# Kernel optimization log

Measured on AMD Instinct MI355X. Metric: run time of the kernel, lower is better.

Reference implementation:

```python
import jax, jax.numpy as jnp
import numpy as np

B, C, NB, H, W = 4, 128, 4, 256, 256
BT = C // NB  # bottleneck channels = 32
BN1_EPS, BN2_EPS = 1e-5, 1e-3


def setup_inputs() -> dict:
    key = jax.random.key(0)
    ks = jax.random.split(key, 16)
    x = jax.random.normal(ks[0], (B, C, H, W), dtype=jnp.float32)
    w1 = jax.random.normal(ks[1], (BT, C), dtype=jnp.float32) * 0.1
    bn1_gamma = 1.0 + 0.1 * jax.random.normal(ks[2], (BT,), dtype=jnp.float32)
    bn1_beta = 0.1 * jax.random.normal(ks[3], (BT,), dtype=jnp.float32)
    bn1_mean = 0.1 * jax.random.normal(ks[4], (BT,), dtype=jnp.float32)
    bn1_var = 0.5 + jax.random.uniform(ks[5], (BT,), dtype=jnp.float32)
    # learned box extents (vertical x, horizontal y), guaranteed x_max > x_min
    x_min = jax.random.uniform(ks[6], (BT, NB), minval=-100.0, maxval=-2.0)
    x_max = x_min + jax.random.uniform(ks[7], (BT, NB), minval=2.0, maxval=100.0)
    y_min = jax.random.uniform(ks[8], (BT, NB), minval=-100.0, maxval=-2.0)
    y_max = y_min + jax.random.uniform(ks[9], (BT, NB), minval=2.0, maxval=100.0)
    bn2_gamma = 1.0 + 0.1 * jax.random.normal(ks[10], (C,), dtype=jnp.float32)
    bn2_beta = 0.1 * jax.random.normal(ks[11], (C,), dtype=jnp.float32)
    bn2_mean = 0.1 * jax.random.normal(ks[12], (C,), dtype=jnp.float32)
    bn2_var = 0.5 + jax.random.uniform(ks[13], (C,), dtype=jnp.float32)
    return dict(x=x, w1=w1, bn1_gamma=bn1_gamma, bn1_beta=bn1_beta,
                bn1_mean=bn1_mean, bn1_var=bn1_var,
                x_min=x_min, x_max=x_max, y_min=y_min, y_max=y_max,
                bn2_gamma=bn2_gamma, bn2_beta=bn2_beta,
                bn2_mean=bn2_mean, bn2_var=bn2_var)


def _bn(z, gamma, beta, mean, var, eps):
    inv = gamma / jnp.sqrt(var + eps)
    return z * inv[None, :, None, None] + (beta - mean * inv)[None, :, None, None]


def _box_conv(z, x_min, x_max, y_min, y_max):
    """Continuous box-average filter via bilinear sampling of the integral image.
    z: (B, BT, H, W); box params: (BT, NB). Output: (B, BT*NB, H, W)."""
    # zero-padded 2D integral image S[b,c,i,j] = sum z[b,c,:i,:j]  -> (B,BT,H+1,W+1)
    S = jnp.pad(jnp.cumsum(jnp.cumsum(z, axis=2), axis=3),
                ((0, 0), (0, 0), (1, 0), (1, 0)))

    def sample(Sc, u, v):
        # Sc: (B,H+1,W+1); u: (H,), v: (W,) continuous coords into the integral image
        u = jnp.clip(u, 0.0, float(H))
        v = jnp.clip(v, 0.0, float(W))
        i0 = jnp.clip(jnp.floor(u), 0.0, float(H - 1)).astype(jnp.int32)
        j0 = jnp.clip(jnp.floor(v), 0.0, float(W - 1)).astype(jnp.int32)
        wu = u - i0  # fractional weights (carry gradients w.r.t. box params)
        wv = v - j0
        R = Sc[:, i0, :] * (1.0 - wu)[None, :, None] + Sc[:, i0 + 1, :] * wu[None, :, None]
        return R[:, :, j0] * (1.0 - wv)[None, None, :] + R[:, :, j0 + 1] * wv[None, None, :]

    def one_box(Sc, xmn, xmx, ymn, ymx):
        i = jnp.arange(H, dtype=z.dtype)
        j = jnp.arange(W, dtype=z.dtype)
        F11 = sample(Sc, i + xmx, j + ymx)
        F10 = sample(Sc, i + xmx, j + ymn)
        F01 = sample(Sc, i + xmn, j + ymx)
        F00 = sample(Sc, i + xmn, j + ymn)
        area = (xmx - xmn) * (ymx - ymn)
        return (F11 - F10 - F01 + F00) / area  # (B,H,W)

    per_box = jax.vmap(one_box, in_axes=(None, 0, 0, 0, 0))     # over NB
    per_chan = jax.vmap(per_box, in_axes=(1, 0, 0, 0, 0))       # over BT channels
    out = per_chan(S, x_min, x_max, y_min, y_max)               # (BT,NB,B,H,W)
    return out.transpose(2, 0, 1, 3, 4).reshape(z.shape[0], BT * NB, H, W)


def reference(x, w1, bn1_gamma, bn1_beta, bn1_mean, bn1_var,
              x_min, x_max, y_min, y_max,
              bn2_gamma, bn2_beta, bn2_mean, bn2_var):
    # 1x1 conv (no bias)
    h = jnp.einsum('bchw,kc->bkhw', x, w1)
    h = _bn(h, bn1_gamma, bn1_beta, bn1_mean, bn1_var, BN1_EPS)
    h = _box_conv(h, x_min, x_max, y_min, y_max)
    h = _bn(h, bn2_gamma, bn2_beta, bn2_mean, bn2_var, BN2_EPS)
    h = jax.nn.relu(h)
    return jax.nn.relu(x + h)
```

## Files before the change

kernel.cpp:

```cpp
#include <hip/hip_runtime.h>
#include <math.h>

#define BB 4
#define CC 128
#define BT 32
#define NBOX 4
#define HH 256
#define WW 256
#define HW (HH*WW)
#define SP 257
#define SPLANE (SP*SP)
#define NPLANE (BB*BT)
#define CHUNK 32
#define NCHUNK (HH/CHUNK)

__global__ __launch_bounds__(256) void conv_bn1(
        const float* __restrict__ x, const float* __restrict__ w1,
        const float* __restrict__ g1, const float* __restrict__ b1,
        const float* __restrict__ m1, const float* __restrict__ v1,
        float* __restrict__ h) {
    int pix = blockIdx.x * 256 + threadIdx.x;
    int b  = pix >> 16;
    int ij = pix & 65535;
    const float* xb = x + b * (CC * HW) + ij;
    float acc[BT];
    #pragma unroll
    for (int k = 0; k < BT; ++k) acc[k] = 0.f;
    #pragma unroll 4
    for (int c = 0; c < CC; ++c) {
        float xv = xb[c * HW];
        #pragma unroll
        for (int k = 0; k < BT; ++k)
            acc[k] = fmaf(xv, w1[k * CC + c], acc[k]);
    }
    float* hb = h + b * (BT * HW) + ij;
    #pragma unroll
    for (int k = 0; k < BT; ++k) {
        float inv = g1[k] * __frsqrt_rn(v1[k] + 1e-5f);
        float add = b1[k] - m1[k] * inv;
        hb[k * HW] = acc[k] * inv + add;
    }
}

__global__ __launch_bounds__(256) void row_scan(float* __restrict__ t) {
    int wave = threadIdx.x >> 6;
    int lane = threadIdx.x & 63;
    int row = blockIdx.x * 4 + wave;
    float4* rp = (float4*)(t + (size_t)row * WW) + lane;
    float4 v = *rp;
    v.y += v.x; v.z += v.y; v.w += v.z;
    float tot = v.w;
    float sum = tot;
    #pragma unroll
    for (int off = 1; off < 64; off <<= 1) {
        float o = __shfl_up(sum, off, 64);
        if (lane >= off) sum += o;
    }
    float excl = sum - tot;
    v.x += excl; v.y += excl; v.z += excl; v.w += excl;
    *rp = v;
}

__global__ __launch_bounds__(256) void col_partial(const float* __restrict__ t,
                                                   float* __restrict__ T) {
    int plane = blockIdx.x >> 3;
    int chunk = blockIdx.x & 7;
    int j = threadIdx.x;
    const float* tp = t + (size_t)plane * HW + chunk * CHUNK * WW + j;
    float s = 0.f;
    #pragma unroll 8
    for (int r = 0; r < CHUNK; ++r) s += tp[r * WW];
    T[blockIdx.x * 256 + j] = s;
}

__global__ __launch_bounds__(256) void col_final(const float* __restrict__ t,
                                                 const float* __restrict__ T,
                                                 float* __restrict__ s) {
    int plane = blockIdx.x >> 3;
    int chunk = blockIdx.x & 7;
    int j = threadIdx.x;
    float off = 0.f;
    for (int c = 0; c < chunk; ++c) off += T[(plane * 8 + c) * 256 + j];
    const float* tp = t + (size_t)plane * HW + chunk * CHUNK * WW + j;
    float* sp = s + (size_t)plane * SPLANE;
    if (chunk == 0) {
        sp[j + 1] = 0.f;
        if (j == 0) sp[0] = 0.f;
    }
    float run = off;
    int rowbase = chunk * CHUNK;
    #pragma unroll 4
    for (int r = 0; r < CHUNK; ++r) {
        run += tp[r * WW];
        sp[(size_t)(rowbase + r + 1) * SP + j + 1] = run;
        if (j == 0) sp[(size_t)(rowbase + r + 1) * SP] = 0.f;
    }
}

__global__ __launch_bounds__(256) void box_sample(
        const float* __restrict__ s, const float* __restrict__ x,
        const float* __restrict__ xmin, const float* __restrict__ xmax,
        const float* __restrict__ ymin, const float* __restrict__ ymax,
        const float* __restrict__ g2, const float* __restrict__ b2,
        const float* __restrict__ m2, const float* __restrict__ v2,
        float* __restrict__ out) {
    __shared__ float D[SP];
    int bid = blockIdx.x;
    int i = bid & 255;
    int n = (bid >> 8) & 3;
    int k = (bid >> 10) & 31;
    int b = bid >> 15;
    int j = threadIdx.x;
    int kn = k * NBOX + n;
    const float* sp = s + (size_t)(b * BT + k) * SPLANE;

    float xmn = xmin[kn], xmx = xmax[kn], ymn = ymin[kn], ymx = ymax[kn];

    float u_hi = fminf(fmaxf((float)i + xmx, 0.f), 256.f);
    float u_lo = fminf(fmaxf((float)i + xmn, 0.f), 256.f);
    int i1 = (int)fminf(floorf(u_hi), 255.f);
    int i0 = (int)fminf(floorf(u_lo), 255.f);
    float wu1 = u_hi - (float)i1;
    float wu0 = u_lo - (float)i0;

    const float* rA = sp + (size_t)i1 * SP;
    const float* rB = rA + SP;
    const float* rC = sp + (size_t)i0 * SP;
    const float* rD = rC + SP;

    D[j] = rA[j] * (1.f - wu1) + rB[j] * wu1 - rC[j] * (1.f - wu0) - rD[j] * wu0;
    if (j == 0)
        D[256] = rA[256] * (1.f - wu1) + rB[256] * wu1
               - rC[256] * (1.f - wu0) - rD[256] * wu0;
    __syncthreads();

    float v_hi = fminf(fmaxf((float)j + ymx, 0.f), 256.f);
    float v_lo = fminf(fmaxf((float)j + ymn, 0.f), 256.f);
    int j1 = (int)fminf(floorf(v_hi), 255.f);
    int j0 = (int)fminf(floorf(v_lo), 255.f);
    float wv1 = v_hi - (float)j1;
    float wv0 = v_lo - (float)j0;

    float hi = D[j1] * (1.f - wv1) + D[j1 + 1] * wv1;
    float lo = D[j0] * (1.f - wv0) + D[j0 + 1] * wv0;

    float inv = g2[kn] * __frsqrt_rn(v2[kn] + 1e-3f);
    float scale = inv * __frcp_rn((xmx - xmn) * (ymx - ymn));
    float add = b2[kn] - m2[kn] * inv;
    float val = (hi - lo) * scale + add;
    val = fmaxf(val, 0.f);
    size_t oidx = ((size_t)(b * CC + kn) * HH + i) * WW + j;
    out[oidx] = fmaxf(x[oidx] + val, 0.f);
}

extern "C" void kernel_launch(void* const* d_in, const int* in_sizes, int n_in,
                              void* d_out, int out_size, void* d_ws, size_t ws_size,
                              hipStream_t stream) {
    const float* x    = (const float*)d_in[0];
    const float* w1   = (const float*)d_in[1];
    const float* g1   = (const float*)d_in[2];
    const float* b1   = (const float*)d_in[3];
    const float* m1   = (const float*)d_in[4];
    const float* v1   = (const float*)d_in[5];
    const float* xmin = (const float*)d_in[6];
    const float* xmax = (const float*)d_in[7];
    const float* ymin = (const float*)d_in[8];
    const float* ymax = (const float*)d_in[9];
    const float* g2   = (const float*)d_in[10];
    const float* b2   = (const float*)d_in[11];
    const float* m2   = (const float*)d_in[12];
    const float* v2   = (const float*)d_in[13];
    float* out = (float*)d_out;

    float* h = (float*)d_ws;
    float* S = h + (size_t)BB * BT * HW;
    float* T = S + (size_t)NPLANE * SPLANE;

    conv_bn1   <<<(BB * HW) / 256, 256, 0, stream>>>(x, w1, g1, b1, m1, v1, h);
    row_scan   <<<BB * BT * HH / 4, 256, 0, stream>>>(h);
    col_partial<<<NPLANE * NCHUNK, 256, 0, stream>>>(h, T);
    col_final  <<<NPLANE * NCHUNK, 256, 0, stream>>>(h, T, S);
    box_sample <<<BB * BT * NBOX * HH, 256, 0, stream>>>(S, x, xmin, xmax, ymin, ymax,
                                                         g2, b2, m2, v2, out);
}
```

Before: 391.3 us.

## Fuse row scan into conv kernel and batch eight rows per box-sample block

The row prefix scan is folded into the 1x1 conv+BN1 kernel. Each 256-thread block covers one image row, so the scan runs as wave shuffles over all 32 channels plus a shared-memory combine of wave totals, which removes one read/write pass over the intermediate. The box-sample kernel now handles 8 output rows per block instead of 1. This cuts the block count and amortises parameter loads, and x and out go through nontemporal loads and stores. The trade-offs are more register pressure and shuffles in the conv kernel and a larger shared-memory buffer in box_sample.

```diff
diff --git a/kernel.cpp b/kernel.cpp
--- a/kernel.cpp
+++ b/kernel.cpp
@@ -13,12 +13,13 @@
 #define NPLANE (BB*BT)
 #define CHUNK 32
 #define NCHUNK (HH/CHUNK)
-
-__global__ __launch_bounds__(256) void conv_bn1(
+#define ROWS 8
+
+__global__ __launch_bounds__(256) void conv_bn1_scan(
         const float* __restrict__ x, const float* __restrict__ w1,
         const float* __restrict__ g1, const float* __restrict__ b1,
         const float* __restrict__ m1, const float* __restrict__ v1,
-        float* __restrict__ h) {
+        float* __restrict__ t) {
     int pix = blockIdx.x * 256 + threadIdx.x;
     int b  = pix >> 16;
     int ij = pix & 65535;
@@ -33,32 +34,37 @@
         for (int k = 0; k < BT; ++k)
             acc[k] = fmaf(xv, w1[k * CC + c], acc[k]);
     }
-    float* hb = h + b * (BT * HW) + ij;
     #pragma unroll
     for (int k = 0; k < BT; ++k) {
         float inv = g1[k] * __frsqrt_rn(v1[k] + 1e-5f);
-        float add = b1[k] - m1[k] * inv;
-        hb[k * HW] = acc[k] * inv + add;
-    }
-}
-
-__global__ __launch_bounds__(256) void row_scan(float* __restrict__ t) {
+        acc[k] = acc[k] * inv + (b1[k] - m1[k] * inv);
+    }
+    int lane = threadIdx.x & 63;
     int wave = threadIdx.x >> 6;
-    int lane = threadIdx.x & 63;
-    int row = blockIdx.x * 4 + wave;
-    float4* rp = (float4*)(t + (size_t)row * WW) + lane;
-    float4 v = *rp;
-    v.y += v.x; v.z += v.y; v.w += v.z;
-    float tot = v.w;
-    float sum = tot;
     #pragma unroll
     for (int off = 1; off < 64; off <<= 1) {
-        float o = __shfl_up(sum, off, 64);
-        if (lane >= off) sum += o;
-    }
-    float excl = sum - tot;
-    v.x += excl; v.y += excl; v.z += excl; v.w += excl;
-    *rp = v;
+        bool p = lane >= off;
+        #pragma unroll
+        for (int k = 0; k < BT; ++k) {
+            float o = __shfl_up(acc[k], off, 64);
+            if (p) acc[k] += o;
+        }
+    }
+    __shared__ float wtot[3][BT];
+    if (lane == 63 && wave < 3) {
+        #pragma unroll
+        for (int k = 0; k < BT; ++k) wtot[wave][k] = acc[k];
+    }
+    __syncthreads();
+    float* tb = t + b * (BT * HW) + ij;
+    #pragma unroll
+    for (int k = 0; k < BT; ++k) {
+        float off = 0.f;
+        if (wave > 0) off += wtot[0][k];
+        if (wave > 1) off += wtot[1][k];
+        if (wave > 2) off += wtot[2][k];
+        tb[k * HW] = acc[k] + off;
+    }
 }
 
 __global__ __launch_bounds__(256) void col_partial(const float* __restrict__ t,
@@ -104,34 +110,47 @@
         const float* __restrict__ g2, const float* __restrict__ b2,
         const float* __restrict__ m2, const float* __restrict__ v2,
         float* __restrict__ out) {
-    __shared__ float D[SP];
+    __shared__ float D[ROWS][SP];
     int bid = blockIdx.x;
-    int i = bid & 255;
-    int n = (bid >> 8) & 3;
-    int k = (bid >> 10) & 31;
-    int b = bid >> 15;
-    int j = threadIdx.x;
+    int ig = bid & 31;
+    int n  = (bid >> 5) & 3;
+    int k  = (bid >> 7) & 31;
+    int b  = bid >> 12;
+    int j  = threadIdx.x;
+    int lane = j & 63;
+    int wave = j >> 6;
     int kn = k * NBOX + n;
+    int ibase = ig * ROWS;
     const float* sp = s + (size_t)(b * BT + k) * SPLANE;
 
     float xmn = xmin[kn], xmx = xmax[kn], ymn = ymin[kn], ymx = ymax[kn];
 
-    float u_hi = fminf(fmaxf((float)i + xmx, 0.f), 256.f);
-    float u_lo = fminf(fmaxf((float)i + xmn, 0.f), 256.f);
-    int i1 = (int)fminf(floorf(u_hi), 255.f);
-    int i0 = (int)fminf(floorf(u_lo), 255.f);
-    float wu1 = u_hi - (float)i1;
-    float wu0 = u_lo - (float)i0;
-
-    const float* rA = sp + (size_t)i1 * SP;
-    const float* rB = rA + SP;
-    const float* rC = sp + (size_t)i0 * SP;
-    const float* rD = rC + SP;
-
-    D[j] = rA[j] * (1.f - wu1) + rB[j] * wu1 - rC[j] * (1.f - wu0) - rD[j] * wu0;
-    if (j == 0)
-        D[256] = rA[256] * (1.f - wu1) + rB[256] * wu1
-               - rC[256] * (1.f - wu0) - rD[256] * wu0;
+    #pragma unroll
+    for (int rr = 0; rr < 2; ++rr) {
+        int r = wave + rr * 4;
+        float fi = (float)(ibase + r);
+        float u_hi = fminf(fmaxf(fi + xmx, 0.f), 256.f);
+        float u_lo = fminf(fmaxf(fi + xmn, 0.f), 256.f);
+        int i1 = (int)fminf(floorf(u_hi), 255.f);
+        int i0 = (int)fminf(floorf(u_lo), 255.f);
+        float wu1 = u_hi - (float)i1;
+        float wu0 = u_lo - (float)i0;
+        const float* rA = sp + (size_t)i1 * SP;
+        const float* rB = rA + SP;
+        const float* rC = sp + (size_t)i0 * SP;
+        const float* rD = rC + SP;
+        #pragma unroll
+        for (int tcol = 0; tcol < 4; ++tcol) {
+            int c = lane + tcol * 64;
+            D[r][c] = rA[c] * (1.f - wu1) + rB[c] * wu1
+                    - rC[c] * (1.f - wu0) - rD[c] * wu0;
+        }
+        if (lane == 0) {
+            int c = 256;
+            D[r][c] = rA[c] * (1.f - wu1) + rB[c] * wu1
+                    - rC[c] * (1.f - wu0) - rD[c] * wu0;
+        }
+    }
     __syncthreads();
 
     float v_hi = fminf(fmaxf((float)j + ymx, 0.f), 256.f);
@@ -140,17 +159,25 @@
     int j0 = (int)fminf(floorf(v_lo), 255.f);
     float wv1 = v_hi - (float)j1;
     float wv0 = v_lo - (float)j0;
-
-    float hi = D[j1] * (1.f - wv1) + D[j1 + 1] * wv1;
-    float lo = D[j0] * (1.f - wv0) + D[j0 + 1] * wv0;
+    float cv1 = 1.f - wv1;
+    float cv0 = 1.f - wv0;
 
     float inv = g2[kn] * __frsqrt_rn(v2[kn] + 1e-3f);
     float scale = inv * __frcp_rn((xmx - xmn) * (ymx - ymn));
     float add = b2[kn] - m2[kn] * inv;
-    float val = (hi - lo) * scale + add;
-    val = fmaxf(val, 0.f);
-    size_t oidx = ((size_t)(b * CC + kn) * HH + i) * WW + j;
-    out[oidx] = fmaxf(x[oidx] + val, 0.f);
+
+    int obase = ((b * CC + kn) * HH + ibase) * WW + j;
+    const float* xp = x + obase;
+    float* op = out + obase;
+    #pragma unroll
+    for (int r = 0; r < ROWS; ++r) {
+        float hi = D[r][j1] * cv1 + D[r][j1 + 1] * wv1;
+        float lo = D[r][j0] * cv0 + D[r][j0 + 1] * wv0;
+        float val = (hi - lo) * scale + add;
+        val = fmaxf(val, 0.f);
+        float xv = __builtin_nontemporal_load(xp + r * WW);
+        __builtin_nontemporal_store(fmaxf(xv + val, 0.f), op + r * WW);
+    }
 }
 
 extern "C" void kernel_launch(void* const* d_in, const int* in_sizes, int n_in,
@@ -176,10 +203,9 @@
     float* S = h + (size_t)BB * BT * HW;
     float* T = S + (size_t)NPLANE * SPLANE;
 
-    conv_bn1   <<<(BB * HW) / 256, 256, 0, stream>>>(x, w1, g1, b1, m1, v1, h);
-    row_scan   <<<BB * BT * HH / 4, 256, 0, stream>>>(h);
-    col_partial<<<NPLANE * NCHUNK, 256, 0, stream>>>(h, T);
-    col_final  <<<NPLANE * NCHUNK, 256, 0, stream>>>(h, T, S);
-    box_sample <<<BB * BT * NBOX * HH, 256, 0, stream>>>(S, x, xmin, xmax, ymin, ymax,
-                                                         g2, b2, m2, v2, out);
-}
+    conv_bn1_scan<<<(BB * HW) / 256, 256, 0, stream>>>(x, w1, g1, b1, m1, v1, h);
+    col_partial  <<<NPLANE * NCHUNK, 256, 0, stream>>>(h, T);
+    col_final    <<<NPLANE * NCHUNK, 256, 0, stream>>>(h, T, S);
+    box_sample   <<<BB * BT * NBOX * (HH / ROWS), 256, 0, stream>>>(
+                     S, x, xmin, xmax, ymin, ymax, g2, b2, m2, v2, out);
+}
```

New measurement: 335.2 us. 1.17x faster.
